# Optimization experiments

Measured on AMD Instinct MI355X. Metric: run time of the kernel, lower is better.

Reference implementation:

```python
import jax, jax.numpy as jnp
import numpy as np
import math

B, S, E, H, L, F, V, MAXLEN = 2, 1024, 1024, 16, 6, 4096, 400, 1024
DH = E // H
PAD_ID = 0


def setup_inputs() -> dict:
    key = jax.random.key(0)
    ks = jax.random.split(key, 12)
    nrm = lambda k, shape, s=0.02: jax.random.normal(k, shape, jnp.float32) * s
    inp = {}
    inp["sequences"] = jax.random.randint(ks[0], (B, S), 3, V + 3)
    inp["map1"] = jax.random.randint(ks[1], (V + 3,), 0, V + 3)
    inp["map2"] = jax.random.randint(ks[2], (V + 3,), 0, V + 3)
    inp["emb"] = nrm(ks[3], (V + 3, E), 1.0)          # nn.Embedding N(0,1)
    inp["pos_emb"] = nrm(ks[4], (MAXLEN + 2, E), 1.0)  # learned positional (torch.randn)
    inp["dist_emb"] = nrm(ks[5], (MAXLEN + 1, H), 0.02)
    inp["in_proj_w"] = nrm(ks[6], (L, 3 * E, E))
    inp["in_proj_b"] = jnp.zeros((L, 3 * E), jnp.float32)
    inp["out_proj_w"] = nrm(ks[7], (L, E, E))
    inp["out_proj_b"] = jnp.zeros((L, E), jnp.float32)
    inp["lin1_w"] = nrm(ks[8], (L, F, E))
    inp["lin1_b"] = jnp.zeros((L, F), jnp.float32)
    inp["lin2_w"] = nrm(ks[9], (L, E, F))
    inp["lin2_b"] = jnp.zeros((L, E), jnp.float32)
    inp["ln1_w"] = jnp.ones((L, E), jnp.float32)
    inp["ln1_b"] = jnp.zeros((L, E), jnp.float32)
    inp["ln2_w"] = jnp.ones((L, E), jnp.float32)
    inp["ln2_b"] = jnp.zeros((L, E), jnp.float32)
    inp["fnorm_w"] = jnp.ones((E,), jnp.float32)
    inp["fnorm_b"] = jnp.zeros((E,), jnp.float32)
    inp["gen_w"] = nrm(ks[10], (V, E))
    inp["gen_b"] = jnp.zeros((V,), jnp.float32)
    return inp


def _layer_norm(x, w, b, eps=1e-5):
    m = x.mean(-1, keepdims=True)
    v = x.var(-1, keepdims=True)
    return (x - m) * jax.lax.rsqrt(v + eps) * w + b


def reference(sequences, map1, map2, emb, pos_emb, dist_emb,
              in_proj_w, in_proj_b, out_proj_w, out_proj_b,
              lin1_w, lin1_b, lin2_w, lin2_b,
              ln1_w, ln1_b, ln2_w, ln2_b,
              fnorm_w, fnorm_b, gen_w, gen_b):
    Bv, Sv = sequences.shape
    # TokenEmbedding: average of two node embeddings, scaled by sqrt(E), + learned pos
    x = (jnp.take(emb, map1[sequences], axis=0) +
         jnp.take(emb, map2[sequences], axis=0)) * (math.sqrt(E) / 2.0)
    x = x + pos_emb[:Sv]  # broadcast over batch
    # Learned relative-position bias + causal mask + key padding
    idx = jnp.arange(Sv)
    dist = jnp.minimum(jnp.abs(idx[None, :] - idx[:, None]), MAXLEN)
    bias = jnp.take(dist_emb, dist, axis=0).transpose(2, 0, 1)  # [H,S,S]
    causal = idx[None, :] <= idx[:, None]                        # key j <= query i
    neg_inf = jnp.float32(-jnp.inf)
    mask = jnp.where(causal[None], bias, neg_inf)                # [H,S,S]
    pad = sequences == PAD_ID                                    # [B,S]
    mask = jnp.where(pad[:, None, None, :], neg_inf, mask[None]) # [B,H,S,S]
    scale = 1.0 / math.sqrt(DH)
    for i in range(L):  # post-norm TransformerEncoderLayer, gelu
        qkv = x @ in_proj_w[i].T + in_proj_b[i]
        q, k, v = jnp.split(qkv, 3, axis=-1)
        q = q.reshape(Bv, Sv, H, DH)
        k = k.reshape(Bv, Sv, H, DH)
        v = v.reshape(Bv, Sv, H, DH)
        scores = jnp.einsum('bihd,bjhd->bhij', q, k) * scale + mask
        attn = jax.nn.softmax(scores, axis=-1)
        ctx = jnp.einsum('bhij,bjhd->bihd', attn, v).reshape(Bv, Sv, E)
        a = ctx @ out_proj_w[i].T + out_proj_b[i]
        x = _layer_norm(x + a, ln1_w[i], ln1_b[i])
        h = jax.nn.gelu(x @ lin1_w[i].T + lin1_b[i], approximate=False)
        ff = h @ lin2_w[i].T + lin2_b[i]
        x = _layer_norm(x + ff, ln2_w[i], ln2_b[i])
    x = _layer_norm(x, fnorm_w, fnorm_b)
    return x @ gen_w.T + gen_b  # [B,S,V]
```

## Files before the change

kernel.cpp:

```cpp
#include <hip/hip_runtime.h>
#include <hip/hip_bf16.h>
#include <math.h>


#define BB 2
#define SS 1024
#define EE 1024
#define HH 16
#define LL 6
#define FF 4096
#define VV 400
#define DH 64
#define STR 68

typedef float f32x4 __attribute__((ext_vector_type(4)));
typedef __bf16 bf16x8 __attribute__((ext_vector_type(8)));
typedef unsigned u32x4 __attribute__((ext_vector_type(4)));

__device__ __forceinline__ unsigned short bf16_bits(float f) {
    union { __bf16 b; unsigned short s; } c; c.b = (__bf16)f; return c.s;
}
__device__ __forceinline__ __bf16 bits_bf16(unsigned short s) {
    union { unsigned short s; __bf16 b; } c; c.s = s; return c.b;
}

__device__ __forceinline__ void split_frag(const f32x4 f0, const f32x4 f1,
                                           bf16x8& h, bf16x8& l)
{
#pragma unroll
    for (int i = 0; i < 4; ++i) {
        float a = f0[i];
        __bf16 ha = (__bf16)a;
        h[i] = ha;
        l[i] = (__bf16)(a - (float)ha);
        float b = f1[i];
        __bf16 hb = (__bf16)b;
        h[i + 4] = hb;
        l[i + 4] = (__bf16)(b - (float)hb);
    }
}

__global__ __launch_bounds__(256) void embed_kernel(
    const int* __restrict__ seq, const int* __restrict__ map1,
    const int* __restrict__ map2, const float* __restrict__ emb,
    const float* __restrict__ pos, float* __restrict__ x)
{
    const int bid = blockIdx.x;
    const int sIdx = bid & (SS - 1);
    const int t = threadIdx.x;
    const int tok = seq[bid];
    const int i1 = map1[tok], i2 = map2[tok];
#pragma unroll
    for (int c = 0; c < 4; ++c) {
        int e = t + c * 256;
        float val = (emb[(size_t)i1 * EE + e] + emb[(size_t)i2 * EE + e]) * 16.0f
                  + pos[(size_t)sIdx * EE + e];
        x[(size_t)bid * EE + e] = val;
    }
}

template <int ACT>
__global__ __launch_bounds__(256) void gemm_nt(
    const float* __restrict__ A, const float* __restrict__ W,
    const float* __restrict__ bias, float* __restrict__ C,
    int M, int N, int K)
{
    __shared__ __align__(16) float As[16][68];
    __shared__ __align__(16) float Wsh[16][68];
    const int t = threadIdx.x;
    const int tx = t & 15, ty = t >> 4;
    const int mBase = blockIdx.y * 64, nBase = blockIdx.x * 64;
    const int lr = t >> 2;
    const int lk = (t & 3) << 2;
    float acc[4][4] = {};
    const float* aPtr = A + (size_t)(mBase + lr) * K + lk;
    const int n = nBase + lr;
    const float* wPtr = W + (size_t)n * K + lk;

    for (int k0 = 0; k0 < K; k0 += 16) {
        float4 av = *(const float4*)(aPtr + k0);
        As[lk + 0][lr] = av.x; As[lk + 1][lr] = av.y;
        As[lk + 2][lr] = av.z; As[lk + 3][lr] = av.w;
        float4 wv = make_float4(0.f, 0.f, 0.f, 0.f);
        if (n < N) wv = *(const float4*)(wPtr + k0);
        Wsh[lk + 0][lr] = wv.x; Wsh[lk + 1][lr] = wv.y;
        Wsh[lk + 2][lr] = wv.z; Wsh[lk + 3][lr] = wv.w;
        __syncthreads();
#pragma unroll
        for (int kk = 0; kk < 16; ++kk) {
            const float4 a = *(const float4*)&As[kk][ty * 4];
            const float4 w = *(const float4*)&Wsh[kk][tx * 4];
            acc[0][0] += a.x * w.x; acc[0][1] += a.x * w.y; acc[0][2] += a.x * w.z; acc[0][3] += a.x * w.w;
            acc[1][0] += a.y * w.x; acc[1][1] += a.y * w.y; acc[1][2] += a.y * w.z; acc[1][3] += a.y * w.w;
            acc[2][0] += a.z * w.x; acc[2][1] += a.z * w.y; acc[2][2] += a.z * w.z; acc[2][3] += a.z * w.w;
            acc[3][0] += a.w * w.x; acc[3][1] += a.w * w.y; acc[3][2] += a.w * w.z; acc[3][3] += a.w * w.w;
        }
        __syncthreads();
    }
#pragma unroll
    for (int i = 0; i < 4; ++i) {
        const int m = mBase + ty * 4 + i;
#pragma unroll
        for (int j = 0; j < 4; ++j) {
            const int nn = nBase + tx * 4 + j;
            if (nn < N) {
                float v = acc[i][j] + bias[nn];
                if (ACT == 1) v = 0.5f * v * (1.0f + erff(v * 0.70710678118654752f));
                C[(size_t)m * N + nn] = v;
            }
        }
    }
}

template <int BM, int BN, int WM, int WN, int ACT>
__global__ __launch_bounds__(256) void gemm_mfma(
    const float* __restrict__ A, const float* __restrict__ W,
    const float* __restrict__ bias, float* __restrict__ C,
    int M, int N, int K)
{
    constexpr int BK = 32;
    constexpr int MF = WM / 16;
    constexpr int NF = WN / 16;
    constexpr int WAVES_N = BN / WN;
    constexpr int TILE = (BM + BN) * BK;
    constexpr int LOADS = BM / 32 + BN / 32;
    static_assert((BM / WM) * WAVES_N == 4, "4 waves per block");

    __shared__ __align__(16) float smem[2 * TILE];

    const int t = threadIdx.x;
    const int wave = t >> 6;
    const int lane = t & 63;
    const int wr = wave / WAVES_N;
    const int wc = wave % WAVES_N;
    const int mBase = blockIdx.y * BM;
    const int nBase = blockIdx.x * BN;

    const int srow = lane >> 3;
    const int schunk = (lane & 7) ^ srow;
    const float* aSrc = A + (size_t)(mBase + srow) * K + schunk * 4;
    const float* wSrc = W + (size_t)(nBase + srow) * K + schunk * 4;

    f32x4 acc[MF][NF];
    const f32x4 zed = {0.f, 0.f, 0.f, 0.f};
#pragma unroll
    for (int i = 0; i < MF; ++i)
#pragma unroll
        for (int j = 0; j < NF; ++j) acc[i][j] = zed;

    const int frow = lane & 15;
    const int c0 = (lane >> 4) << 1;

#define STAGE(bufptr, k0)                                                     \
    {                                                                          \
        float* As_ = (bufptr);                                                 \
        float* Ws_ = (bufptr) + BM * BK;                                       \
        _Pragma("unroll")                                                      \
        for (int i = 0; i < BM / 32; ++i)                                      \
            __builtin_amdgcn_global_load_lds(                                  \
                (const __attribute__((address_space(1))) void*)                \
                    (aSrc + (size_t)(i * 32 + wave * 8) * K + (k0)),           \
                (__attribute__((address_space(3))) void*)                      \
                    ((char*)As_ + (i * 4 + wave) * 1024), 16, 0, 0);           \
        _Pragma("unroll")                                                      \
        for (int i = 0; i < BN / 32; ++i)                                      \
            __builtin_amdgcn_global_load_lds(                                  \
                (const __attribute__((address_space(1))) void*)                \
                    (wSrc + (size_t)(i * 32 + wave * 8) * K + (k0)),           \
                (__attribute__((address_space(3))) void*)                      \
                    ((char*)Ws_ + (i * 4 + wave) * 1024), 16, 0, 0);           \
    }

#define COMPUTE(bufptr)                                                        \
    {                                                                          \
        const float* As_ = (bufptr);                                           \
        const float* Ws_ = (bufptr) + BM * BK;                                 \
        bf16x8 ah[MF], al[MF], bh[NF], bl[NF];                                 \
        _Pragma("unroll")                                                      \
        for (int i = 0; i < MF; ++i) {                                         \
            const int r = wr * WM + i * 16 + frow;                             \
            const int s = r & 7;                                               \
            const float* base = As_ + r * BK;                                  \
            f32x4 f0 = *(const f32x4*)(base + ((c0 ^ s) << 2));                \
            f32x4 f1 = *(const f32x4*)(base + (((c0 + 1) ^ s) << 2));          \
            split_frag(f0, f1, ah[i], al[i]);                                  \
        }                                                                      \
        _Pragma("unroll")                                                      \
        for (int j = 0; j < NF; ++j) {                                         \
            const int r = wc * WN + j * 16 + frow;                             \
            const int s = r & 7;                                               \
            const float* base = Ws_ + r * BK;                                  \
            f32x4 f0 = *(const f32x4*)(base + ((c0 ^ s) << 2));                \
            f32x4 f1 = *(const f32x4*)(base + (((c0 + 1) ^ s) << 2));          \
            split_frag(f0, f1, bh[j], bl[j]);                                  \
        }                                                                      \
        _Pragma("unroll")                                                      \
        for (int i = 0; i < MF; ++i)                                           \
            _Pragma("unroll")                                                  \
            for (int j = 0; j < NF; ++j) {                                     \
                acc[i][j] = __builtin_amdgcn_mfma_f32_16x16x32_bf16(ah[i], bh[j], acc[i][j], 0, 0, 0); \
                acc[i][j] = __builtin_amdgcn_mfma_f32_16x16x32_bf16(ah[i], bl[j], acc[i][j], 0, 0, 0); \
                acc[i][j] = __builtin_amdgcn_mfma_f32_16x16x32_bf16(al[i], bh[j], acc[i][j], 0, 0, 0); \
            }                                                                  \
    }

    const int NT = K / BK;
    STAGE(smem, 0);
    int cur = 0;
    for (int tt = 0; tt < NT - 1; ++tt) {
        float* curBuf = smem + cur * TILE;
        float* nxtBuf = smem + (cur ^ 1) * TILE;
        STAGE(nxtBuf, (tt + 1) * BK);
        asm volatile("s_waitcnt vmcnt(%0)" :: "n"(LOADS) : "memory");
        __builtin_amdgcn_s_barrier();
        COMPUTE(curBuf);
        asm volatile("s_waitcnt lgkmcnt(0)" ::: "memory");
        __builtin_amdgcn_s_barrier();
        cur ^= 1;
    }
    {
        float* curBuf = smem + cur * TILE;
        asm volatile("s_waitcnt vmcnt(0)" ::: "memory");
        __builtin_amdgcn_s_barrier();
        COMPUTE(curBuf);
    }
#undef STAGE
#undef COMPUTE

    const int crow = (lane >> 4) << 2;
    const int ccol = lane & 15;
#pragma unroll
    for (int i = 0; i < MF; ++i) {
        const int row = mBase + wr * WM + i * 16 + crow;
#pragma unroll
        for (int j = 0; j < NF; ++j) {
            const int col = nBase + wc * WN + j * 16 + ccol;
            const float bv = bias[col];
            float* cp = C + (size_t)row * N + col;
#pragma unroll
            for (int r = 0; r < 4; ++r) {
                float v = acc[i][j][r] + bv;
                if (ACT == 1) v = 0.5f * v * (1.0f + erff(v * 0.70710678118654752f));
                cp[(size_t)r * N] = v;
            }
        }
    }
}

__global__ __launch_bounds__(256) void fattn_mfma(
    const float* __restrict__ qkv, const float* __restrict__ dist_emb,
    float* __restrict__ ctx)
{
    __shared__ __align__(16) float Ks[64][68];
    __shared__ __align__(16) float Vt[64][68];
    __shared__ __align__(16) unsigned PsHL[4][16][68];
    __shared__ float bias_l[1024];

    const int t = threadIdx.x;
    const int wave = t >> 6, lane = t & 63;
    const int x = lane & 15, g = lane >> 4;
    const int bid = blockIdx.x;
    const int b  = bid >> 8;
    const int h  = (bid >> 4) & (HH - 1);
    int qt = bid & 15;
    if (b & 1) qt = 15 - qt;
    const int i0 = qt * 64;

    for (int d = t; d < 1024; d += 256) bias_l[d] = dist_emb[d * HH + h];

    bf16x8 qh[2], ql[2];
    {
        const float* qp = qkv + (size_t)(b * SS + i0 + wave * 16 + x) * (3 * EE)
                          + h * DH + g * 8;
        f32x4 a0 = *(const f32x4*)qp;
        f32x4 a1 = *(const f32x4*)(qp + 4);
        split_frag(a0, a1, qh[0], ql[0]);
        f32x4 b0 = *(const f32x4*)(qp + 32);
        f32x4 b1 = *(const f32x4*)(qp + 36);
        split_frag(b0, b1, qh[1], ql[1]);
    }

    const f32x4 zed = {0.f, 0.f, 0.f, 0.f};
    f32x4 O[4] = {zed, zed, zed, zed};
    float m_reg[4] = {-INFINITY, -INFINITY, -INFINITY, -INFINITY};
    float l_reg[4] = {0.f, 0.f, 0.f, 0.f};

    const int krow0 = t >> 4;
    const int kch   = (t & 15) * 4;
    const int vd    = t & 63;
    const int sV    = (vd ^ (vd >> 3)) & 7;

    float4 kreg[4], vreg[4];
#define LOAD_TILE(j0_)                                                         \
    {                                                                          \
        _Pragma("unroll")                                                      \
        for (int c = 0; c < 4; ++c) {                                          \
            const int row = krow0 + 16 * c;                                    \
            kreg[c] = *(const float4*)(qkv + (size_t)(b * SS + (j0_) + row) * (3 * EE) \
                                       + EE + h * DH + kch);                   \
            const int rc = (t >> 6) + 4 * c;                                   \
            const float* vb = qkv + (size_t)(b * SS + (j0_) + rc * 4) * (3 * EE) \
                              + 2 * EE + h * DH + vd;                          \
            vreg[c].x = vb[0];                                                 \
            vreg[c].y = vb[3 * EE];                                            \
            vreg[c].z = vb[6 * EE];                                            \
            vreg[c].w = vb[9 * EE];                                            \
        }                                                                      \
    }

    LOAD_TILE(0);

    for (int kt = 0; kt <= qt; ++kt) {
        __syncthreads();
#pragma unroll
        for (int c = 0; c < 4; ++c) {
            *(float4*)&Ks[krow0 + 16 * c][kch] = kreg[c];
            const int rc = (t >> 6) + 4 * c;
            *(float4*)&Vt[vd][(rc ^ sV) * 4] = vreg[c];
        }
        __syncthreads();
        if (kt < qt) LOAD_TILE((kt + 1) * 64);

        f32x4 sacc[4] = {zed, zed, zed, zed};
#pragma unroll
        for (int ks = 0; ks < 2; ++ks) {
#pragma unroll
            for (int j = 0; j < 4; ++j) {
                const int r = j * 16 + x;
                f32x4 f0 = *(const f32x4*)&Ks[r][ks * 32 + g * 8];
                f32x4 f1 = *(const f32x4*)&Ks[r][ks * 32 + g * 8 + 4];
                bf16x8 kh, kl;
                split_frag(f0, f1, kh, kl);
                sacc[j] = __builtin_amdgcn_mfma_f32_16x16x32_bf16(qh[ks], kh, sacc[j], 0, 0, 0);
                sacc[j] = __builtin_amdgcn_mfma_f32_16x16x32_bf16(qh[ks], kl, sacc[j], 0, 0, 0);
                sacc[j] = __builtin_amdgcn_mfma_f32_16x16x32_bf16(ql[ks], kh, sacc[j], 0, 0, 0);
            }
        }

        const int j0 = kt * 64;
        const int qrow = i0 + wave * 16 + g * 4;
        float pv[4][4], mt[4];
#pragma unroll
        for (int r = 0; r < 4; ++r) mt[r] = -INFINITY;
#pragma unroll
        for (int j = 0; j < 4; ++j) {
            const int jg = j0 + j * 16 + x;
#pragma unroll
            for (int r = 0; r < 4; ++r) {
                const int dd = qrow + r - jg;
                float v = (dd < 0) ? -INFINITY
                                   : sacc[j][r] * 0.125f + bias_l[dd];
                pv[j][r] = v;
                mt[r] = fmaxf(mt[r], v);
            }
        }
#pragma unroll
        for (int r = 0; r < 4; ++r)
#pragma unroll
            for (int msk = 1; msk <= 8; msk <<= 1)
                mt[r] = fmaxf(mt[r], __shfl_xor(mt[r], msk));
        float alpha[4], lsum[4];
#pragma unroll
        for (int r = 0; r < 4; ++r) {
            const float mnew = fmaxf(m_reg[r], mt[r]);
            alpha[r] = __expf(m_reg[r] - mnew);
            m_reg[r] = mnew;
            lsum[r] = 0.f;
        }
#pragma unroll
        for (int j = 0; j < 4; ++j)
#pragma unroll
            for (int r = 0; r < 4; ++r) {
                float p = __expf(pv[j][r] - m_reg[r]);
                pv[j][r] = p;
                lsum[r] += p;
            }
#pragma unroll
        for (int r = 0; r < 4; ++r) {
#pragma unroll
            for (int msk = 1; msk <= 8; msk <<= 1)
                lsum[r] += __shfl_xor(lsum[r], msk);
            l_reg[r] = l_reg[r] * alpha[r] + lsum[r];
            O[0][r] *= alpha[r]; O[1][r] *= alpha[r];
            O[2][r] *= alpha[r]; O[3][r] *= alpha[r];
        }

#pragma unroll
        for (int j = 0; j < 4; ++j)
#pragma unroll
            for (int r = 0; r < 4; ++r) {
                float p = pv[j][r];
                unsigned short hs = bf16_bits(p);
                unsigned short ls = bf16_bits(p - (float)bits_bf16(hs));
                PsHL[wave][g * 4 + r][j * 16 + x] = (unsigned)hs | ((unsigned)ls << 16);
            }

#pragma unroll
        for (int ks = 0; ks < 2; ++ks) {
            const unsigned* pp = &PsHL[wave][x][ks * 32 + g * 8];
            u32x4 pa = *(const u32x4*)pp;
            u32x4 pb = *(const u32x4*)(pp + 4);
            bf16x8 ph, pl;
#pragma unroll
            for (int i2 = 0; i2 < 4; ++i2) {
                ph[i2] = bits_bf16((unsigned short)(pa[i2] & 0xffff));
                pl[i2] = bits_bf16((unsigned short)(pa[i2] >> 16));
                ph[i2 + 4] = bits_bf16((unsigned short)(pb[i2] & 0xffff));
                pl[i2 + 4] = bits_bf16((unsigned short)(pb[i2] >> 16));
            }
#pragma unroll
            for (int j = 0; j < 4; ++j) {
                const int d = j * 16 + x;
                const int sv = (d ^ (d >> 3)) & 7;
                const int c0 = ks * 8 + g * 2;
                f32x4 f0 = *(const f32x4*)&Vt[d][(c0 ^ sv) * 4];
                f32x4 f1 = *(const f32x4*)&Vt[d][((c0 + 1) ^ sv) * 4];
                bf16x8 vh, vl;
                split_frag(f0, f1, vh, vl);
                O[j] = __builtin_amdgcn_mfma_f32_16x16x32_bf16(ph, vh, O[j], 0, 0, 0);
                O[j] = __builtin_amdgcn_mfma_f32_16x16x32_bf16(ph, vl, O[j], 0, 0, 0);
                O[j] = __builtin_amdgcn_mfma_f32_16x16x32_bf16(pl, vh, O[j], 0, 0, 0);
            }
        }
    }
#undef LOAD_TILE

#pragma unroll
    for (int r = 0; r < 4; ++r) {
        const float linv = 1.0f / l_reg[r];
        float* cp = ctx + (size_t)(b * SS + i0 + wave * 16 + g * 4 + r) * EE
                    + h * DH + x;
#pragma unroll
        for (int j = 0; j < 4; ++j) cp[j * 16] = O[j][r] * linv;
    }
}

__global__ __launch_bounds__(256) void add_ln_kernel(
    float* __restrict__ x, const float* __restrict__ a,
    const float* __restrict__ w, const float* __restrict__ bb, int hasAdd)
{
    __shared__ float red[8];
    const int row = blockIdx.x, t = threadIdx.x;
    float v[4]; float s = 0.f, ss = 0.f;
#pragma unroll
    for (int c = 0; c < 4; ++c) {
        int e = t + c * 256;
        float val = x[(size_t)row * EE + e];
        if (hasAdd) val += a[(size_t)row * EE + e];
        v[c] = val; s += val; ss += val * val;
    }
#pragma unroll
    for (int o = 32; o > 0; o >>= 1) { s += __shfl_down(s, o); ss += __shfl_down(ss, o); }
    if ((t & 63) == 0) { red[t >> 6] = s; red[4 + (t >> 6)] = ss; }
    __syncthreads();
    s  = red[0] + red[1] + red[2] + red[3];
    ss = red[4] + red[5] + red[6] + red[7];
    const float mean = s * (1.0f / EE);
    const float var  = ss * (1.0f / EE) - mean * mean;
    const float inv  = rsqrtf(var + 1e-5f);
#pragma unroll
    for (int c = 0; c < 4; ++c) {
        int e = t + c * 256;
        x[(size_t)row * EE + e] = (v[c] - mean) * inv * w[e] + bb[e];
    }
}

extern "C" void kernel_launch(void* const* d_in, const int* in_sizes, int n_in,
                              void* d_out, int out_size, void* d_ws, size_t ws_size,
                              hipStream_t stream)
{
    const int*   seq       = (const int*)d_in[0];
    const int*   map1      = (const int*)d_in[1];
    const int*   map2      = (const int*)d_in[2];
    const float* emb       = (const float*)d_in[3];
    const float* pos_emb   = (const float*)d_in[4];
    const float* dist_emb  = (const float*)d_in[5];
    const float* in_proj_w = (const float*)d_in[6];
    const float* in_proj_b = (const float*)d_in[7];
    const float* out_proj_w= (const float*)d_in[8];
    const float* out_proj_b= (const float*)d_in[9];
    const float* lin1_w    = (const float*)d_in[10];
    const float* lin1_b    = (const float*)d_in[11];
    const float* lin2_w    = (const float*)d_in[12];
    const float* lin2_b    = (const float*)d_in[13];
    const float* ln1_w     = (const float*)d_in[14];
    const float* ln1_b     = (const float*)d_in[15];
    const float* ln2_w     = (const float*)d_in[16];
    const float* ln2_b     = (const float*)d_in[17];
    const float* fnorm_w   = (const float*)d_in[18];
    const float* fnorm_b   = (const float*)d_in[19];
    const float* gen_w     = (const float*)d_in[20];
    const float* gen_b     = (const float*)d_in[21];

    float* ws   = (float*)d_ws;
    float* x    = ws;
    float* qkv  = ws + 2097152;
    float* ctx  = ws + 8388608;
    float* t2   = ws + 10485760;
    float* hbuf = ws + 12582912;

    const int M = BB * SS;
    dim3 blk(256);

    embed_kernel<<<M, blk, 0, stream>>>(seq, map1, map2, emb, pos_emb, x);

    for (int l = 0; l < LL; ++l) {
        gemm_mfma<64, 128, 32, 64, 0><<<dim3((3 * EE) / 128, M / 64), blk, 0, stream>>>(
            x, in_proj_w + (size_t)l * 3 * EE * EE, in_proj_b + (size_t)l * 3 * EE,
            qkv, M, 3 * EE, EE);
        fattn_mfma<<<BB * HH * (SS / 64), blk, 0, stream>>>(qkv, dist_emb, ctx);
        gemm_mfma<64, 128, 32, 64, 0><<<dim3(EE / 128, M / 64), blk, 0, stream>>>(
            ctx, out_proj_w + (size_t)l * EE * EE, out_proj_b + (size_t)l * EE,
            t2, M, EE, EE);
        add_ln_kernel<<<M, blk, 0, stream>>>(x, t2, ln1_w + (size_t)l * EE, ln1_b + (size_t)l * EE, 1);
        gemm_mfma<128, 128, 64, 64, 1><<<dim3(FF / 128, M / 128), blk, 0, stream>>>(
            x, lin1_w + (size_t)l * FF * EE, lin1_b + (size_t)l * FF,
            hbuf, M, FF, EE);
        gemm_mfma<64, 128, 32, 64, 0><<<dim3(EE / 128, M / 64), blk, 0, stream>>>(
            hbuf, lin2_w + (size_t)l * EE * FF, lin2_b + (size_t)l * EE,
            t2, M, EE, FF);
        add_ln_kernel<<<M, blk, 0, stream>>>(x, t2, ln2_w + (size_t)l * EE, ln2_b + (size_t)l * EE, 1);
    }
    add_ln_kernel<<<M, blk, 0, stream>>>(x, nullptr, fnorm_w, fnorm_b, 0);
    gemm_nt<0><<<dim3((VV + 63) / 64, M / 64), blk, 0, stream>>>(
        x, gen_w, gen_b, (float*)d_out, M, VV, EE);
}
```

Measured before the change: 2.434 ms.

## Pre-split weights into bf16 hi/lo arrays and use split GEMM kernel

Adds a kernel that splits each fp32 weight matrix once per call into bf16 high and low halves in workspace. A new GEMM variant loads these pre-split halves straight into LDS, so weight tiles no longer need per-tile fp32-to-bf16 splitting and move half as many bytes per array. This adds a split pass over all layer weights each call, needs more workspace, and only runs when the workspace is large enough.

```diff
diff --git a/kernel.cpp b/kernel.cpp
--- a/kernel.cpp
+++ b/kernel.cpp
@@ -37,6 +37,25 @@
         __bf16 hb = (__bf16)b;
         h[i + 4] = hb;
         l[i + 4] = (__bf16)(b - (float)hb);
+    }
+}
+
+__global__ __launch_bounds__(256) void split_kernel(
+    const float* __restrict__ w, unsigned short* __restrict__ hi,
+    unsigned short* __restrict__ lo, int n4)
+{
+    int idx = blockIdx.x * 256 + threadIdx.x;
+    const int stride = gridDim.x * 256;
+    for (int i = idx; i < n4; i += stride) {
+        float4 v = ((const float4*)w)[i];
+        ushort4 hv, lv;
+        float f;
+        f = v.x; hv.x = bf16_bits(f); lv.x = bf16_bits(f - (float)bits_bf16(hv.x));
+        f = v.y; hv.y = bf16_bits(f); lv.y = bf16_bits(f - (float)bits_bf16(hv.y));
+        f = v.z; hv.z = bf16_bits(f); lv.z = bf16_bits(f - (float)bits_bf16(hv.z));
+        f = v.w; hv.w = bf16_bits(f); lv.w = bf16_bits(f - (float)bits_bf16(hv.w));
+        ((ushort4*)hi)[i] = hv;
+        ((ushort4*)lo)[i] = lv;
     }
 }
 
@@ -226,6 +245,155 @@
     }
 #undef STAGE
 #undef COMPUTE
+
+    const int crow = (lane >> 4) << 2;
+    const int ccol = lane & 15;
+#pragma unroll
+    for (int i = 0; i < MF; ++i) {
+        const int row = mBase + wr * WM + i * 16 + crow;
+#pragma unroll
+        for (int j = 0; j < NF; ++j) {
+            const int col = nBase + wc * WN + j * 16 + ccol;
+            const float bv = bias[col];
+            float* cp = C + (size_t)row * N + col;
+#pragma unroll
+            for (int r = 0; r < 4; ++r) {
+                float v = acc[i][j][r] + bv;
+                if (ACT == 1) v = 0.5f * v * (1.0f + erff(v * 0.70710678118654752f));
+                cp[(size_t)r * N] = v;
+            }
+        }
+    }
+}
+
+template <int BM, int BN, int WM, int WN, int ACT>
+__global__ __launch_bounds__(256) void gemm_sw(
+    const float* __restrict__ A, const unsigned short* __restrict__ Wh,
+    const unsigned short* __restrict__ Wl,
+    const float* __restrict__ bias, float* __restrict__ C,
+    int M, int N, int K)
+{
+    constexpr int BK = 32;
+    constexpr int MF = WM / 16;
+    constexpr int NF = WN / 16;
+    constexpr int WAVES_N = BN / WN;
+    constexpr int ABYTES = BM * BK * 4;
+    constexpr int WBYTES = BN * BK * 2;
+    constexpr int TILEB = ABYTES + 2 * WBYTES;
+    constexpr int LOADS = BM / 32 + 2 * (BN / 64);
+    static_assert((BM / WM) * WAVES_N == 4, "4 waves per block");
+
+    __shared__ __align__(16) char smem[2 * TILEB];
+
+    const int t = threadIdx.x;
+    const int wave = t >> 6;
+    const int lane = t & 63;
+    const int wr = wave / WAVES_N;
+    const int wc = wave % WAVES_N;
+    const int mBase = blockIdx.y * BM;
+    const int nBase = blockIdx.x * BN;
+
+    const int arow = lane >> 3;
+    const int achunk = (lane & 7) ^ arow;
+    const float* aSrc = A + (size_t)(mBase + arow) * K + achunk * 4;
+
+    const int wrow = lane >> 2;
+    const int wchunk = (lane & 3) ^ ((wrow ^ (wrow >> 2)) & 3);
+    const size_t wlanoff = (size_t)wrow * K + wchunk * 8;
+
+    f32x4 acc[MF][NF];
+    const f32x4 zed = {0.f, 0.f, 0.f, 0.f};
+#pragma unroll
+    for (int i = 0; i < MF; ++i)
+#pragma unroll
+        for (int j = 0; j < NF; ++j) acc[i][j] = zed;
+
+    const int frow = lane & 15;
+    const int g = lane >> 4;
+
+#define STAGE_SW(bufofs, k0)                                                   \
+    {                                                                          \
+        char* base_ = smem + (bufofs);                                         \
+        _Pragma("unroll")                                                      \
+        for (int i = 0; i < BM / 32; ++i)                                      \
+            __builtin_amdgcn_global_load_lds(                                  \
+                (const __attribute__((address_space(1))) void*)                \
+                    (aSrc + (size_t)(i * 32 + wave * 8) * K + (k0)),           \
+                (__attribute__((address_space(3))) void*)                      \
+                    (base_ + (i * 4 + wave) * 1024), 16, 0, 0);                \
+        _Pragma("unroll")                                                      \
+        for (int i = 0; i < BN / 64; ++i) {                                    \
+            const int wi = wave * (BN / 64) + i;                               \
+            __builtin_amdgcn_global_load_lds(                                  \
+                (const __attribute__((address_space(1))) void*)                \
+                    (Wh + (size_t)(nBase + wi * 16) * K + wlanoff + (k0)),     \
+                (__attribute__((address_space(3))) void*)                      \
+                    (base_ + ABYTES + wi * 1024), 16, 0, 0);                   \
+            __builtin_amdgcn_global_load_lds(                                  \
+                (const __attribute__((address_space(1))) void*)                \
+                    (Wl + (size_t)(nBase + wi * 16) * K + wlanoff + (k0)),     \
+                (__attribute__((address_space(3))) void*)                      \
+                    (base_ + ABYTES + WBYTES + wi * 1024), 16, 0, 0);          \
+        }                                                                      \
+    }
+
+#define COMPUTE_SW(bufofs)                                                     \
+    {                                                                          \
+        const char* base_ = smem + (bufofs);                                   \
+        const float* As_ = (const float*)base_;                                \
+        const char* WhB_ = base_ + ABYTES;                                     \
+        const char* WlB_ = base_ + ABYTES + WBYTES;                            \
+        bf16x8 ah[MF], al[MF], bh[NF], bl[NF];                                 \
+        _Pragma("unroll")                                                      \
+        for (int i = 0; i < MF; ++i) {                                         \
+            const int r = wr * WM + i * 16 + frow;                             \
+            const int s = r & 7;                                               \
+            const float* rb = As_ + r * BK;                                    \
+            const int c0 = g * 2;                                              \
+            f32x4 f0 = *(const f32x4*)(rb + ((c0 ^ s) << 2));                  \
+            f32x4 f1 = *(const f32x4*)(rb + (((c0 + 1) ^ s) << 2));            \
+            split_frag(f0, f1, ah[i], al[i]);                                  \
+        }                                                                      \
+        _Pragma("unroll")                                                      \
+        for (int j = 0; j < NF; ++j) {                                         \
+            const int r = wc * WN + j * 16 + frow;                             \
+            const int s2 = (r ^ (r >> 2)) & 3;                                 \
+            const int pc = g ^ s2;                                             \
+            bh[j] = *(const bf16x8*)(WhB_ + r * 64 + pc * 16);                 \
+            bl[j] = *(const bf16x8*)(WlB_ + r * 64 + pc * 16);                 \
+        }                                                                      \
+        _Pragma("unroll")                                                      \
+        for (int i = 0; i < MF; ++i)                                           \
+            _Pragma("unroll")                                                  \
+            for (int j = 0; j < NF; ++j) {                                     \
+                acc[i][j] = __builtin_amdgcn_mfma_f32_16x16x32_bf16(ah[i], bh[j], acc[i][j], 0, 0, 0); \
+                acc[i][j] = __builtin_amdgcn_mfma_f32_16x16x32_bf16(ah[i], bl[j], acc[i][j], 0, 0, 0); \
+                acc[i][j] = __builtin_amdgcn_mfma_f32_16x16x32_bf16(al[i], bh[j], acc[i][j], 0, 0, 0); \
+            }                                                                  \
+    }
+
+    const int NT = K / BK;
+    STAGE_SW(0, 0);
+    int cur = 0;
+    for (int tt = 0; tt < NT - 1; ++tt) {
+        const int curOfs = cur * TILEB;
+        const int nxtOfs = (cur ^ 1) * TILEB;
+        STAGE_SW(nxtOfs, (tt + 1) * BK);
+        asm volatile("s_waitcnt vmcnt(%0)" :: "n"(LOADS) : "memory");
+        __builtin_amdgcn_s_barrier();
+        COMPUTE_SW(curOfs);
+        asm volatile("s_waitcnt lgkmcnt(0)" ::: "memory");
+        __builtin_amdgcn_s_barrier();
+        cur ^= 1;
+    }
+    {
+        const int curOfs = cur * TILEB;
+        asm volatile("s_waitcnt vmcnt(0)" ::: "memory");
+        __builtin_amdgcn_s_barrier();
+        COMPUTE_SW(curOfs);
+    }
+#undef STAGE_SW
+#undef COMPUTE_SW
 
     const int crow = (lane >> 4) << 2;
     const int ccol = lane & 15;
@@ -499,26 +667,66 @@
     float* t2   = ws + 10485760;
     float* hbuf = ws + 12582912;
 
+    const size_t IPN = (size_t)LL * 3 * EE * EE;
+    const size_t OPN = (size_t)LL * EE * EE;
+    const size_t L1N = (size_t)LL * FF * EE;
+    const size_t L2N = (size_t)LL * EE * FF;
+    unsigned short* wsp = (unsigned short*)(ws + 20971520);
+    unsigned short* iph = wsp;                 unsigned short* ipl = iph + IPN;
+    unsigned short* oph = ipl + IPN;           unsigned short* opl = oph + OPN;
+    unsigned short* l1h = opl + OPN;           unsigned short* l1l = l1h + L1N;
+    unsigned short* l2h = l1l + L1N;           unsigned short* l2l = l2h + L2N;
+    const size_t needed = 20971520ull * 4 + 2ull * (IPN + OPN + L1N + L2N) * 2;
+    const bool use_split = ws_size >= needed;
+
     const int M = BB * SS;
     dim3 blk(256);
 
+    if (use_split) {
+        split_kernel<<<1024, blk, 0, stream>>>(in_proj_w,  iph, ipl, (int)(IPN / 4));
+        split_kernel<<<1024, blk, 0, stream>>>(out_proj_w, oph, opl, (int)(OPN / 4));
+        split_kernel<<<1024, blk, 0, stream>>>(lin1_w,     l1h, l1l, (int)(L1N / 4));
+        split_kernel<<<1024, blk, 0, stream>>>(lin2_w,     l2h, l2l, (int)(L2N / 4));
+    }
+
     embed_kernel<<<M, blk, 0, stream>>>(seq, map1, map2, emb, pos_emb, x);
 
     for (int l = 0; l < LL; ++l) {
-        gemm_mfma<64, 128, 32, 64, 0><<<dim3((3 * EE) / 128, M / 64), blk, 0, stream>>>(
-            x, in_proj_w + (size_t)l * 3 * EE * EE, in_proj_b + (size_t)l * 3 * EE,
-            qkv, M, 3 * EE, EE);
+        if (use_split) {
+            gemm_sw<64, 128, 32, 64, 0><<<dim3((3 * EE) / 128, M / 64), blk, 0, stream>>>(
+                x, iph + (size_t)l * 3 * EE * EE, ipl + (size_t)l * 3 * EE * EE,
+                in_proj_b + (size_t)l * 3 * EE, qkv, M, 3 * EE, EE);
+        } else {
+            gemm_mfma<64, 128, 32, 64, 0><<<dim3((3 * EE) / 128, M / 64), blk, 0, stream>>>(
+                x, in_proj_w + (size_t)l * 3 * EE * EE, in_proj_b + (size_t)l * 3 * EE,
+                qkv, M, 3 * EE, EE);
+        }
         fattn_mfma<<<BB * HH * (SS / 64), blk, 0, stream>>>(qkv, dist_emb, ctx);
-        gemm_mfma<64, 128, 32, 64, 0><<<dim3(EE / 128, M / 64), blk, 0, stream>>>(
-            ctx, out_proj_w + (size_t)l * EE * EE, out_proj_b + (size_t)l * EE,
-            t2, M, EE, EE);
+        if (use_split) {
+            gemm_sw<64, 128, 32, 64, 0><<<dim3(EE / 128, M / 64), blk, 0, stream>>>(
+                ctx, oph + (size_t)l * EE * EE, opl + (size_t)l * EE * EE,
+                out_proj_b + (size_t)l * EE, t2, M, EE, EE);
+        } else {
+            gemm_mfma<64, 128, 32, 64, 0><<<dim3(EE / 128, M / 64), blk, 0, stream>>>(
+                ctx, out_proj_w + (size_t)l * EE * EE, out_proj_b + (size_t)l * EE,
+                t2, M, EE, EE);
+        }
         add_ln_kernel<<<M, blk, 0, stream>>>(x, t2, ln1_w + (size_t)l * EE, ln1_b + (size_t)l * EE, 1);
-        gemm_mfma<128, 128, 64, 64, 1><<<dim3(FF / 128, M / 128), blk, 0, stream>>>(
-            x, lin1_w + (size_t)l * FF * EE, lin1_b + (size_t)l * FF,
-            hbuf, M, FF, EE);
-        gemm_mfma<64, 128, 32, 64, 0><<<dim3(EE / 128, M / 64), blk, 0, stream>>>(
-            hbuf, lin2_w + (size_t)l * EE * FF, lin2_b + (size_t)l * EE,
-            t2, M, EE, FF);
+        if (use_split) {
+            gemm_sw<128, 128, 64, 64, 1><<<dim3(FF / 128, M / 128), blk, 0, stream>>>(
+                x, l1h + (size_t)l * FF * EE, l1l + (size_t)l * FF * EE,
+                lin1_b + (size_t)l * FF, hbuf, M, FF, EE);
+            gemm_sw<64, 128, 32, 64, 0><<<dim3(EE / 128, M / 64), blk, 0, stream>>>(
+                hbuf, l2h + (size_t)l * EE * FF, l2l + (size_t)l * EE * FF,
+                lin2_b + (size_t)l * EE, t2, M, EE, FF);
+        } else {
+            gemm_mfma<128, 128, 64, 64, 1><<<dim3(FF / 128, M / 128), blk, 0, stream>>>(
+                x, lin1_w + (size_t)l * FF * EE, lin1_b + (size_t)l * FF,
+                hbuf, M, FF, EE);
+            gemm_mfma<64, 128, 32, 64, 0><<<dim3(EE / 128, M / 64), blk, 0, stream>>>(
+                hbuf, lin2_w + (size_t)l * EE * FF, lin2_b + (size_t)l * EE,
+                t2, M, EE, FF);
+        }
         add_ln_kernel<<<M, blk, 0, stream>>>(x, t2, ln2_w + (size_t)l * EE, ln2_b + (size_t)l * EE, 1);
     }
     add_ln_kernel<<<M, blk, 0, stream>>>(x, nullptr, fnorm_w, fnorm_b, 0);
```

After: 2.365 ms. 1.03x faster.
